# Kernel tuning notes

Measured on AMD Instinct MI355X. Metric: run time of the kernel, lower is better.

The kernel has to match this reference:

```python
import jax, jax.numpy as jnp
import numpy as np

N_IN, M_MID = 512, 256
B, H, W = 16, 64, 64

def setup_inputs() -> dict:
    key = jax.random.key(0)
    ks = jax.random.split(key, 7)
    s = 0.05
    return {
        "x": jax.random.normal(ks[0], (B, N_IN, H, W), dtype=jnp.float32),
        "W_state": jax.random.normal(ks[1], (M_MID, N_IN), dtype=jnp.float32) * s,
        "b_state": jax.random.normal(ks[2], (M_MID,), dtype=jnp.float32) * s,
        "W_proj": jax.random.normal(ks[3], (M_MID, N_IN), dtype=jnp.float32) * s,
        "b_proj": jax.random.normal(ks[4], (M_MID,), dtype=jnp.float32) * s,
        "W_extend": jax.random.normal(ks[5], (N_IN, M_MID), dtype=jnp.float32) * s,
        "b_extend": jax.random.normal(ks[6], (N_IN,), dtype=jnp.float32) * s,
    }

def reference(x, W_state, b_state, W_proj, b_proj, W_extend, b_extend):
    n, c, h, w = x.shape
    hw = h * w
    xf = x.reshape(n, c, hw)                                   # [n, C, HW]
    # 1x1 convs are channel GEMMs over flattened spatial dim
    x_state = jnp.einsum('mc,nch->nmh', W_state, xf) + b_state[None, :, None]   # [n, M, HW]
    x_proj = jnp.einsum('mc,nch->nmh', W_proj, xf) + b_proj[None, :, None]      # [n, M, HW]
    # bmm -> scale -> softmax -> bmm (graph reasoning over M x M)
    scores = jnp.einsum('nmh,nkh->nmk', x_state, x_proj) / jnp.sqrt(jnp.float32(hw))
    attn = jax.nn.softmax(scores, axis=2)                      # [n, M, M]
    x_rstate = jnp.einsum('nmk,nkh->nmh', attn, x_proj)        # [n, M, HW]
    # extend back to C channels + residual
    ext = jnp.einsum('cm,nmh->nch', W_extend, x_rstate) + b_extend[None, :, None]
    return x + ext.reshape(n, c, h, w)
```

## Files before the change

### kernel.cpp

```cpp
#include <hip/hip_runtime.h>
#include <hip/hip_bf16.h>
#include <stdint.h>

typedef __bf16 bf16x8_t __attribute__((ext_vector_type(8)));
typedef float  f32x4_t  __attribute__((ext_vector_type(4)));
typedef short  short8_t __attribute__((ext_vector_type(8)));

__device__ __forceinline__ unsigned short f2b(float f) {
    union { float f; unsigned u; } v; v.f = f;
    unsigned u = v.u;
    return (unsigned short)((u + 0x7FFFu + ((u >> 16) & 1u)) >> 16);
}
__device__ __forceinline__ float b2f(unsigned short b) {
    union { unsigned u; float f; } v; v.u = ((unsigned)b) << 16; return v.f;
}

#define AS3(p) ((__attribute__((address_space(3))) void*)(p))
#define AS1(p) ((const __attribute__((address_space(1))) void*)(p))
#define FENCE() asm volatile("" ::: "memory")

#define NB   16
#define CIN  512
#define MMID 256
#define HW   4096
#define KSPLIT 8
#define ASZ  (128 * 64)
#define ASZ2 (256 * 64)

__device__ __forceinline__ void swz3(int gx, int gy, int& bx, int& by, int& bz) {
    const int nwg = gridDim.x, ord = blockIdx.x, q = nwg >> 3;
    const int s = (ord & 7) * q + (ord >> 3);
    by = s % gy;
    const int rem = s / gy;
    bx = rem % gx;
    bz = rem / gx;
}

__global__ __launch_bounds__(256) void prep_weights(
    const float* __restrict__ Ws, const float* __restrict__ Wp,
    const float* __restrict__ Wef, const float* __restrict__ bs,
    const float* __restrict__ bp,
    unsigned short* __restrict__ Wsp, unsigned short* __restrict__ Wex,
    unsigned short* __restrict__ WpT, float* __restrict__ bsp)
{
    int i = blockIdx.x * 256 + threadIdx.x;
    if (i < MMID * CIN) {
        Wsp[i]              = f2b(Ws[i]);
        Wsp[MMID * CIN + i] = f2b(Wp[i]);
        Wex[i]              = f2b(Wef[i]);
        const int c = i >> 8, k = i & (MMID - 1);
        WpT[i] = f2b(Wp[(size_t)k * CIN + c]);
    }
    if (i < MMID) { bsp[i] = bs[i]; bsp[MMID + i] = bp[i]; }
}

__global__ __launch_bounds__(256) void transpose_convert_x(
    const float* __restrict__ x, unsigned short* __restrict__ xT)
{
    __shared__ unsigned short tile[64][66];
    const int n = blockIdx.z, c0 = blockIdx.y * 64, h0 = blockIdx.x * 64;
    const float* s = x + ((size_t)n * CIN + c0) * HW + h0;
    unsigned short* d = xT + ((size_t)n * HW + h0) * CIN + c0;
    const int t = threadIdx.x;
    {
        const int rr = t >> 4, cc = (t & 15) * 4;
        #pragma unroll
        for (int p = 0; p < 4; ++p) {
            int r = p * 16 + rr;
            float4 v = *(const float4*)(s + (size_t)r * HW + cc);
            tile[r][cc + 0] = f2b(v.x); tile[r][cc + 1] = f2b(v.y);
            tile[r][cc + 2] = f2b(v.z); tile[r][cc + 3] = f2b(v.w);
        }
    }
    __syncthreads();
    {
        const int wr = t >> 3, wc = (t & 7) * 8;
        #pragma unroll
        for (int p = 0; p < 2; ++p) {
            int h = p * 32 + wr;
            unsigned short tmp[8];
            #pragma unroll
            for (int j = 0; j < 8; ++j) tmp[j] = tile[wc + j][h];
            *(short8_t*)(d + (size_t)h * CIN + wc) = *(const short8_t*)tmp;
        }
    }
}

__global__ __launch_bounds__(256) void transpose_bf16_64(
    const unsigned short* __restrict__ src, unsigned short* __restrict__ dst,
    int srs, int drs, long long sbs, long long dbs)
{
    __shared__ unsigned short tile[64][66];
    const int n = blockIdx.z, r0 = blockIdx.y * 64, c0 = blockIdx.x * 64;
    const unsigned short* s = src + (size_t)n * sbs + (size_t)r0 * srs + c0;
    unsigned short* d = dst + (size_t)n * dbs + (size_t)c0 * drs + r0;
    const int t = threadIdx.x;
    const int rr = t >> 3, cc = (t & 7) * 8;
    #pragma unroll
    for (int p = 0; p < 2; ++p) {
        int r = p * 32 + rr;
        short8_t v = *(const short8_t*)(s + (size_t)r * srs + cc);
        #pragma unroll
        for (int j = 0; j < 8; ++j) tile[r][cc + j] = ((const unsigned short*)&v)[j];
    }
    __syncthreads();
    #pragma unroll
    for (int p = 0; p < 2; ++p) {
        int c = p * 32 + rr;
        unsigned short tmp[8];
        #pragma unroll
        for (int j = 0; j < 8; ++j) tmp[j] = tile[cc + j][c];
        *(short8_t*)(d + (size_t)c * drs + cc) = *(const short8_t*)tmp;
    }
}

template <int EPI>
__device__ __forceinline__ void epilogue_repack(
    f32x4_t (&acc)[4][4], unsigned short* smem,
    int m0, int n0, int wave, int lane,
    const float* __restrict__ bias, const float* __restrict__ resid,
    void* __restrict__ Cout, int ldc, size_t cbase)
{
    float* fbuf = (float*)smem;
    const int t   = wave * 64 + lane;
    const int l15 = lane & 15, l16 = lane >> 4;
    const int wr2 = wave >> 1;
    const int wc  = (wave & 1) * 64;

    #pragma unroll
    for (int p = 0; p < 4; ++p) {
        __syncthreads();
        if (wr2 == (p >> 1)) {
            const int ihalf = p & 1;
            #pragma unroll
            for (int i2 = 0; i2 < 2; ++i2) {
                const int i = ihalf * 2 + i2;
                #pragma unroll
                for (int r = 0; r < 4; ++r) {
                    const int lrow = i2 * 16 + l16 * 4 + r;
                    #pragma unroll
                    for (int j = 0; j < 4; ++j)
                        fbuf[lrow * 132 + wc + j * 16 + l15] = acc[i][j][r];
                }
            }
        }
        __syncthreads();
        #pragma unroll
        for (int it = 0; it < 2; ++it) {
            const int lrow = it * 16 + (t >> 4);
            const int col  = (t & 15) * 8;
            const int row  = m0 + p * 32 + lrow;
            float v[8];
            *(float4*)&v[0] = *(const float4*)&fbuf[lrow * 132 + col];
            *(float4*)&v[4] = *(const float4*)&fbuf[lrow * 132 + col + 4];
            float badd = 0.f;
            if constexpr (EPI == 0 || EPI == 3) badd = bias[row];
            const size_t idx = cbase + (size_t)row * ldc + n0 + col;
            if constexpr (EPI == 3) {
                float o[8];
                const float* rp = resid + idx;
                float4 r0 = *(const float4*)rp;
                float4 r1 = *(const float4*)(rp + 4);
                o[0] = v[0] + badd + r0.x; o[1] = v[1] + badd + r0.y;
                o[2] = v[2] + badd + r0.z; o[3] = v[3] + badd + r0.w;
                o[4] = v[4] + badd + r1.x; o[5] = v[5] + badd + r1.y;
                o[6] = v[6] + badd + r1.z; o[7] = v[7] + badd + r1.w;
                float* op = (float*)Cout + idx;
                *(float4*)op = *(const float4*)&o[0];
                *(float4*)(op + 4) = *(const float4*)&o[4];
            } else if constexpr (EPI == 1) {
                float* op = (float*)Cout + idx;
                *(float4*)op = *(const float4*)&v[0];
                *(float4*)(op + 4) = *(const float4*)&v[4];
            } else {
                unsigned short o[8];
                #pragma unroll
                for (int k = 0; k < 8; ++k) o[k] = f2b(v[k] + badd);
                *(short8_t*)((unsigned short*)Cout + idx) = *(const short8_t*)o;
            }
        }
    }
}

#define GEMM_KLOOP(Ab, Bb, lda, ldb, KBEG, NT)                                          \
    auto stage = [&](int k0, int b) {                                                   \
        unsigned short* Asb = smem + b * 2 * ASZ;                                       \
        unsigned short* Bsb = Asb + ASZ;                                                \
        _Pragma("unroll")                                                               \
        for (int c = 0; c < 4; ++c) {                                                   \
            const int o   = (c * 256 + t) * 16;                                         \
            const int row = o >> 7;                                                     \
            const int ce  = ((o & 127) ^ ((row & 7) << 4)) >> 1;                        \
            __builtin_amdgcn_global_load_lds(                                           \
                AS1(Ab + (size_t)row * lda + k0 + ce), AS3((char*)Asb + o), 16, 0, 0);  \
            __builtin_amdgcn_global_load_lds(                                           \
                AS1(Bb + (size_t)row * ldb + k0 + ce), AS3((char*)Bsb + o), 16, 0, 0);  \
        }                                                                               \
    };                                                                                  \
    stage(KBEG, 0);                                                                     \
    for (int itk = 0; itk < (NT); ++itk) {                                              \
        const int cur = itk & 1;                                                        \
        if (itk + 1 < (NT)) {                                                           \
            stage(KBEG + (itk + 1) * 64, cur ^ 1);                                      \
            asm volatile("s_waitcnt vmcnt(8)" ::: "memory");                            \
        } else {                                                                        \
            asm volatile("s_waitcnt vmcnt(0)" ::: "memory");                            \
        }                                                                               \
        __builtin_amdgcn_s_barrier();                                                   \
        FENCE();                                                                        \
        const char* Asb = (const char*)(smem + cur * 2 * ASZ);                          \
        const char* Bsb = Asb + 2 * ASZ;                                                \
        const int swz = (l15 & 7) << 4;                                                 \
        _Pragma("unroll")                                                               \
        for (int ks = 0; ks < 2; ++ks) {                                                \
            bf16x8_t af[4], bfr[4];                                                     \
            const int cb = (ks * 64 + l16 * 16) ^ swz;                                  \
            _Pragma("unroll")                                                           \
            for (int i = 0; i < 4; ++i) {                                               \
                af[i]  = *(const bf16x8_t*)(Asb + (wr + i * 16 + l15) * 128 + cb);      \
                bfr[i] = *(const bf16x8_t*)(Bsb + (wc + i * 16 + l15) * 128 + cb);      \
            }                                                                           \
            _Pragma("unroll")                                                           \
            for (int i = 0; i < 4; ++i)                                                 \
                _Pragma("unroll")                                                       \
                for (int j = 0; j < 4; ++j)                                             \
                    acc[i][j] = __builtin_amdgcn_mfma_f32_16x16x32_bf16(                \
                        af[i], bfr[j], acc[i][j], 0, 0, 0);                             \
        }                                                                               \
        FENCE();                                                                        \
        __builtin_amdgcn_s_barrier();                                                   \
        FENCE();                                                                        \
    }

template <int EPI>
__global__ __launch_bounds__(512, 2) void gemm256(
    const unsigned short* __restrict__ A, const unsigned short* __restrict__ B,
    int lda, int ldb, int K,
    long long strideA, long long strideB,
    const float* __restrict__ bias, int bias_bstride,
    const float* __restrict__ resid,
    void* __restrict__ Cout, int ldc, long long strideC,
    int gx, int gy)
{
    __shared__ unsigned short smem[4 * ASZ2];

    int bx, by, n;  swz3(gx, gy, bx, by, n);
    const int m0 = by * 256;
    const int n0 = bx * 256;

    const unsigned short* Ab = A + (size_t)n * strideA + (size_t)m0 * lda;
    const unsigned short* Bb = B + (size_t)n * strideB + (size_t)n0 * ldb;

    const int t    = threadIdx.x;
    const int lane = t & 63;
    const int wave = t >> 6;
    const int wr2  = wave >> 2;
    const int wc4  = wave & 3;
    const int l15  = lane & 15;
    const int l16  = lane >> 4;

    f32x4_t acc[8][4] = {};

    auto stage = [&](int k0, int b) {
        unsigned short* Asb = smem + b * 2 * ASZ2;
        unsigned short* Bsb = Asb + ASZ2;
        #pragma unroll
        for (int c = 0; c < 4; ++c) {
            const int o   = (c * 512 + t) * 16;
            const int row = o >> 7;
            const int ce  = ((o & 127) ^ ((row & 7) << 4)) >> 1;
            __builtin_amdgcn_global_load_lds(
                AS1(Ab + (size_t)row * lda + k0 + ce), AS3((char*)Asb + o), 16, 0, 0);
            __builtin_amdgcn_global_load_lds(
                AS1(Bb + (size_t)row * ldb + k0 + ce), AS3((char*)Bsb + o), 16, 0, 0);
        }
    };

    const int NT = K / 64;
    stage(0, 0);
    for (int itk = 0; itk < NT; ++itk) {
        const int cur = itk & 1;
        if (itk + 1 < NT) {
            stage((itk + 1) * 64, cur ^ 1);
            asm volatile("s_waitcnt vmcnt(8)" ::: "memory");
        } else {
            asm volatile("s_waitcnt vmcnt(0)" ::: "memory");
        }
        __builtin_amdgcn_s_barrier();
        FENCE();
        const char* Asb = (const char*)(smem + cur * 2 * ASZ2);
        const char* Bsb = Asb + 2 * ASZ2;
        const int swz = (l15 & 7) << 4;
        #pragma unroll
        for (int ks = 0; ks < 2; ++ks) {
            const int cb = (ks * 64 + l16 * 16) ^ swz;
            bf16x8_t af[8], bfr[4];
            #pragma unroll
            for (int i = 0; i < 8; ++i)
                af[i] = *(const bf16x8_t*)(Asb + (wr2 * 128 + i * 16 + l15) * 128 + cb);
            #pragma unroll
            for (int j = 0; j < 4; ++j)
                bfr[j] = *(const bf16x8_t*)(Bsb + (wc4 * 64 + j * 16 + l15) * 128 + cb);
            #pragma unroll
            for (int i = 0; i < 8; ++i)
                #pragma unroll
                for (int j = 0; j < 4; ++j)
                    acc[i][j] = __builtin_amdgcn_mfma_f32_16x16x32_bf16(
                        af[i], bfr[j], acc[i][j], 0, 0, 0);
        }
        FENCE();
        __builtin_amdgcn_s_barrier();
        FENCE();
    }

    float* fbuf = (float*)smem;
    const size_t cbase = (size_t)n * strideC;
    const float* beff = bias ? bias + (size_t)n * bias_bstride : nullptr;
    #pragma unroll
    for (int p = 0; p < 8; ++p) {
        __syncthreads();
        if (wr2 == (p >> 2)) {
            #pragma unroll
            for (int i2 = 0; i2 < 2; ++i2) {
                const int i = (p & 3) * 2 + i2;
                #pragma unroll
                for (int r = 0; r < 4; ++r) {
                    const int lrow = i2 * 16 + l16 * 4 + r;
                    #pragma unroll
                    for (int j = 0; j < 4; ++j)
                        fbuf[lrow * 264 + wc4 * 64 + j * 16 + l15] = acc[i][j][r];
                }
            }
        }
        __syncthreads();
        #pragma unroll
        for (int it = 0; it < 2; ++it) {
            const int lrow = it * 16 + (t >> 5);
            const int col  = (t & 31) * 8;
            const int row  = m0 + p * 32 + lrow;
            float v[8];
            *(float4*)&v[0] = *(const float4*)&fbuf[lrow * 264 + col];
            *(float4*)&v[4] = *(const float4*)&fbuf[lrow * 264 + col + 4];
            const float badd = beff ? beff[row] : 0.f;
            const size_t idx = cbase + (size_t)row * ldc + n0 + col;
            if constexpr (EPI == 3) {
                float o[8];
                const float* rp = resid + idx;
                float4 r0 = *(const float4*)rp;
                float4 r1 = *(const float4*)(rp + 4);
                o[0] = v[0] + badd + r0.x; o[1] = v[1] + badd + r0.y;
                o[2] = v[2] + badd + r0.z; o[3] = v[3] + badd + r0.w;
                o[4] = v[4] + badd + r1.x; o[5] = v[5] + badd + r1.y;
                o[6] = v[6] + badd + r1.z; o[7] = v[7] + badd + r1.w;
                float* op = (float*)Cout + idx;
                *(float4*)op = *(const float4*)&o[0];
                *(float4*)(op + 4) = *(const float4*)&o[4];
            } else {
                unsigned short o[8];
                #pragma unroll
                for (int k = 0; k < 8; ++k) o[k] = f2b(v[k] + badd);
                *(short8_t*)((unsigned short*)Cout + idx) = *(const short8_t*)o;
            }
        }
    }
}

__global__ __launch_bounds__(256) void gemm_scores(
    const unsigned short* __restrict__ Ysp, float* __restrict__ scoresP)
{
    __shared__ unsigned short smem[4 * ASZ];

    int bx, by, z;  swz3(MMID / 128, MMID / 128, bx, by, z);
    const int n  = z >> 3;
    const int kc = z & 7;
    const int m0 = by * 128;
    const int n0 = bx * 128;

    const unsigned short* Ab = Ysp + (size_t)n * CIN * HW + (size_t)m0 * HW;
    const unsigned short* Bb = Ysp + (size_t)n * CIN * HW + (size_t)(MMID + n0) * HW;

    const int t    = threadIdx.x;
    const int lane = t & 63;
    const int wave = t >> 6;
    const int wr   = (wave >> 1) * 64;
    const int wc   = (wave & 1) * 64;
    const int l15  = lane & 15;
    const int l16  = lane >> 4;

    f32x4_t acc[4][4] = {};
    const int kbeg = kc * (HW / KSPLIT);
    GEMM_KLOOP(Ab, Bb, HW, HW, kbeg, (HW / KSPLIT) / 64)

    float* outp = scoresP + (size_t)(kc * NB + n) * MMID * MMID;
    epilogue_repack<1>(acc, smem, m0, n0, wave, lane, nullptr, nullptr,
                       outp, MMID, 0);
}

__global__ __launch_bounds__(256) void softmax_rows(
    const float* __restrict__ scoresP, unsigned short* __restrict__ attn)
{
    const int wave = threadIdx.x >> 6;
    const int l    = threadIdx.x & 63;
    const size_t row = (size_t)blockIdx.x * 4 + wave;
    const size_t pstride = (size_t)NB * MMID * MMID;
    float4 v = {0.f, 0.f, 0.f, 0.f};
    #pragma unroll
    for (int p = 0; p < KSPLIT; ++p) {
        float4 u = *(const float4*)(scoresP + p * pstride + row * MMID + l * 4);
        v.x += u.x; v.y += u.y; v.z += u.z; v.w += u.w;
    }
    float mx = fmaxf(fmaxf(v.x, v.y), fmaxf(v.z, v.w));
    #pragma unroll
    for (int off = 32; off; off >>= 1) mx = fmaxf(mx, __shfl_xor(mx, off));
    const float sc = 0.015625f;
    float e0 = __expf((v.x - mx) * sc), e1 = __expf((v.y - mx) * sc);
    float e2 = __expf((v.z - mx) * sc), e3 = __expf((v.w - mx) * sc);
    float sum = e0 + e1 + e2 + e3;
    #pragma unroll
    for (int off = 32; off; off >>= 1) sum += __shfl_xor(sum, off);
    const float inv = 1.0f / sum;
    unsigned short o[4] = { f2b(e0 * inv), f2b(e1 * inv), f2b(e2 * inv), f2b(e3 * inv) };
    *(uint64_t*)(attn + row * MMID + l * 4) = *(const uint64_t*)o;
}

__global__ __launch_bounds__(256) void compute_vec(
    const unsigned short* __restrict__ G, const float* __restrict__ bsp,
    const float* __restrict__ be, float* __restrict__ vec)
{
    const int n = blockIdx.x >> 1;
    const int c = ((blockIdx.x & 1) << 8) + threadIdx.x;
    const unsigned short* g = G + ((size_t)n * CIN + c) * MMID;
    float s = 0.f;
    for (int k = 0; k < MMID; k += 8) {
        short8_t v = *(const short8_t*)(g + k);
        #pragma unroll
        for (int j = 0; j < 8; ++j)
            s += b2f((unsigned short)v[j]) * bsp[MMID + k + j];
    }
    vec[n * CIN + c] = be[c] + s;
}

template <int EPI>
__global__ __launch_bounds__(256) void gemm_nt(
    const unsigned short* __restrict__ A, const unsigned short* __restrict__ B,
    int lda, int ldb, int K,
    long long strideA, long long strideB,
    const float* __restrict__ bias, int bias_bstride,
    const float* __restrict__ resid,
    void* __restrict__ Cout, int ldc, long long strideC,
    int gx, int gy)
{
    __shared__ unsigned short smem[4 * ASZ];

    int bx, by, n;  swz3(gx, gy, bx, by, n);
    const int m0 = by * 128;
    const int n0 = bx * 128;

    const unsigned short* Ab = A + (size_t)n * strideA + (size_t)m0 * lda;
    const unsigned short* Bb = B + (size_t)n * strideB + (size_t)n0 * ldb;

    const int t    = threadIdx.x;
    const int lane = t & 63;
    const int wave = t >> 6;
    const int wr   = (wave >> 1) * 64;
    const int wc   = (wave & 1) * 64;
    const int l15  = lane & 15;
    const int l16  = lane >> 4;

    f32x4_t acc[4][4] = {};
    GEMM_KLOOP(Ab, Bb, lda, ldb, 0, K / 64)

    const float* beff = bias ? bias + (size_t)n * bias_bstride : nullptr;
    epilogue_repack<EPI>(acc, smem, m0, n0, wave, lane, beff, resid,
                         Cout, ldc, (size_t)n * strideC);
}

extern "C" void kernel_launch(void* const* d_in, const int* in_sizes, int n_in,
                              void* d_out, int out_size, void* d_ws, size_t ws_size,
                              hipStream_t stream)
{
    const float* x   = (const float*)d_in[0];
    const float* Ws  = (const float*)d_in[1];
    const float* bs  = (const float*)d_in[2];
    const float* Wp  = (const float*)d_in[3];
    const float* bp  = (const float*)d_in[4];
    const float* Wef = (const float*)d_in[5];
    const float* be  = (const float*)d_in[6];
    float* out = (float*)d_out;

    unsigned short* xT   = (unsigned short*)d_ws;
    unsigned short* Ysp  = xT   + (size_t)NB * HW * CIN;
    unsigned short* Wsp  = Ysp  + (size_t)NB * CIN * HW;
    unsigned short* Wex  = Wsp  + (size_t)CIN * CIN;
    unsigned short* WpT  = Wex  + (size_t)CIN * MMID;
    unsigned short* attn = WpT  + (size_t)CIN * MMID;
    unsigned short* attnT= attn + (size_t)NB * MMID * MMID;
    unsigned short* G    = attnT+ (size_t)NB * MMID * MMID;
    unsigned short* Meff = G    + (size_t)NB * CIN * MMID;
    float* scoresP = (float*)(Meff + (size_t)NB * CIN * CIN);
    float* bsp = scoresP + (size_t)KSPLIT * NB * MMID * MMID;
    float* vec = bsp + CIN;

    prep_weights<<<512, 256, 0, stream>>>(Ws, Wp, Wef, bs, bp, Wsp, Wex, WpT, bsp);

    transpose_convert_x<<<dim3(HW / 64, CIN / 64, NB), 256, 0, stream>>>(x, xT);

    gemm256<0><<<(HW / 256) * (CIN / 256) * NB, 512, 0, stream>>>(
        Wsp, xT, CIN, CIN, CIN,
        0LL, (long long)HW * CIN,
        bsp, 0, nullptr, Ysp, HW, (long long)CIN * HW,
        HW / 256, CIN / 256);

    gemm_scores<<<(MMID / 128) * (MMID / 128) * NB * KSPLIT, 256, 0, stream>>>(
        Ysp, scoresP);

    softmax_rows<<<NB * MMID / 4, 256, 0, stream>>>(scoresP, attn);

    transpose_bf16_64<<<dim3(MMID / 64, MMID / 64, NB), 256, 0, stream>>>(
        attn, attnT, MMID, MMID, (long long)MMID * MMID, (long long)MMID * MMID);

    gemm_nt<2><<<(MMID / 128) * (CIN / 128) * NB, 256, 0, stream>>>(
        Wex, attnT, MMID, MMID, MMID,
        0LL, (long long)MMID * MMID,
        nullptr, 0, nullptr, G, MMID, (long long)CIN * MMID,
        MMID / 128, CIN / 128);

    compute_vec<<<NB * 2, 256, 0, stream>>>(G, bsp, be, vec);

    gemm_nt<2><<<(CIN / 128) * (CIN / 128) * NB, 256, 0, stream>>>(
        G, WpT, MMID, MMID, MMID,
        (long long)CIN * MMID, 0LL,
        nullptr, 0, nullptr, Meff, CIN, (long long)CIN * CIN,
        CIN / 128, CIN / 128);

    gemm256<3><<<(HW / 256) * (CIN / 256) * NB, 512, 0, stream>>>(
        Meff, xT, CIN, CIN, CIN,
        (long long)CIN * CIN, (long long)HW * CIN,
        vec, CIN, x, out, HW, (long long)CIN * HW,
        HW / 256, CIN / 256);
}
```

Baseline: 224.2 us.

## Use full-M 512x128 GEMM tiles and fold residual into identity-augmented Meff

Replaces the 256x256 batched GEMM with a 512x128 tile that covers the whole output-channel dimension, so each block streams its xT column tile only once. The residual add is moved into the effective matrix by adding the identity in the Meff epilogue, which removes the fp32 x read from the final GEMM epilogue. The score GEMM split-K is also halved. In exchange the residual now passes through bf16 (Meff+I rounded, xT in bf16), which lowers accuracy, and occupancy drops to one block per CU because of the larger LDS footprint.

```diff
diff --git a/kernel.cpp b/kernel.cpp
--- a/kernel.cpp
+++ b/kernel.cpp
@@ -23,9 +23,10 @@
 #define CIN  512
 #define MMID 256
 #define HW   4096
-#define KSPLIT 8
+#define KSPLIT 4
 #define ASZ  (128 * 64)
-#define ASZ2 (256 * 64)
+#define ASZA (512 * 64)
+#define ASZB (128 * 64)
 
 __device__ __forceinline__ void swz3(int gx, int gy, int& bx, int& by, int& bz) {
     const int nwg = gridDim.x, ord = blockIdx.x, q = nwg >> 3;
@@ -118,7 +119,6 @@
 __device__ __forceinline__ void epilogue_repack(
     f32x4_t (&acc)[4][4], unsigned short* smem,
     int m0, int n0, int wave, int lane,
-    const float* __restrict__ bias, const float* __restrict__ resid,
     void* __restrict__ Cout, int ldc, size_t cbase)
 {
     float* fbuf = (float*)smem;
@@ -153,29 +153,21 @@
             float v[8];
             *(float4*)&v[0] = *(const float4*)&fbuf[lrow * 132 + col];
             *(float4*)&v[4] = *(const float4*)&fbuf[lrow * 132 + col + 4];
-            float badd = 0.f;
-            if constexpr (EPI == 0 || EPI == 3) badd = bias[row];
             const size_t idx = cbase + (size_t)row * ldc + n0 + col;
-            if constexpr (EPI == 3) {
-                float o[8];
-                const float* rp = resid + idx;
-                float4 r0 = *(const float4*)rp;
-                float4 r1 = *(const float4*)(rp + 4);
-                o[0] = v[0] + badd + r0.x; o[1] = v[1] + badd + r0.y;
-                o[2] = v[2] + badd + r0.z; o[3] = v[3] + badd + r0.w;
-                o[4] = v[4] + badd + r1.x; o[5] = v[5] + badd + r1.y;
-                o[6] = v[6] + badd + r1.z; o[7] = v[7] + badd + r1.w;
-                float* op = (float*)Cout + idx;
-                *(float4*)op = *(const float4*)&o[0];
-                *(float4*)(op + 4) = *(const float4*)&o[4];
-            } else if constexpr (EPI == 1) {
+            if constexpr (EPI == 1) {
                 float* op = (float*)Cout + idx;
                 *(float4*)op = *(const float4*)&v[0];
                 *(float4*)(op + 4) = *(const float4*)&v[4];
+            } else if constexpr (EPI == 4) {
+                unsigned short o[8];
+                #pragma unroll
+                for (int k = 0; k < 8; ++k)
+                    o[k] = f2b(v[k] + ((row == n0 + col + k) ? 1.0f : 0.0f));
+                *(short8_t*)((unsigned short*)Cout + idx) = *(const short8_t*)o;
             } else {
                 unsigned short o[8];
                 #pragma unroll
-                for (int k = 0; k < 8; ++k) o[k] = f2b(v[k] + badd);
+                for (int k = 0; k < 8; ++k) o[k] = f2b(v[k]);
                 *(short8_t*)((unsigned short*)Cout + idx) = *(const short8_t*)o;
             }
         }
@@ -233,63 +225,65 @@
     }
 
 template <int EPI>
-__global__ __launch_bounds__(512, 2) void gemm256(
+__global__ __launch_bounds__(512, 1) void gemm512(
     const unsigned short* __restrict__ A, const unsigned short* __restrict__ B,
-    int lda, int ldb, int K,
     long long strideA, long long strideB,
     const float* __restrict__ bias, int bias_bstride,
-    const float* __restrict__ resid,
-    void* __restrict__ Cout, int ldc, long long strideC,
-    int gx, int gy)
-{
-    __shared__ unsigned short smem[4 * ASZ2];
-
-    int bx, by, n;  swz3(gx, gy, bx, by, n);
-    const int m0 = by * 256;
-    const int n0 = bx * 256;
-
-    const unsigned short* Ab = A + (size_t)n * strideA + (size_t)m0 * lda;
-    const unsigned short* Bb = B + (size_t)n * strideB + (size_t)n0 * ldb;
+    void* __restrict__ Cout, int ldc, long long strideC, int gx)
+{
+    __shared__ unsigned short smem[2 * (ASZA + ASZB)];
+
+    int bx, by, n;  swz3(gx, 1, bx, by, n);
+    const int n0 = bx * 128;
+
+    const unsigned short* Ab = A + (size_t)n * strideA;
+    const unsigned short* Bb = B + (size_t)n * strideB + (size_t)n0 * CIN;
 
     const int t    = threadIdx.x;
     const int lane = t & 63;
     const int wave = t >> 6;
-    const int wr2  = wave >> 2;
-    const int wc4  = wave & 3;
+    const int wr   = (wave >> 1) * 128;
+    const int wc   = (wave & 1) * 64;
     const int l15  = lane & 15;
     const int l16  = lane >> 4;
 
     f32x4_t acc[8][4] = {};
 
     auto stage = [&](int k0, int b) {
-        unsigned short* Asb = smem + b * 2 * ASZ2;
-        unsigned short* Bsb = Asb + ASZ2;
-        #pragma unroll
-        for (int c = 0; c < 4; ++c) {
+        unsigned short* Asb = smem + b * (ASZA + ASZB);
+        unsigned short* Bsb = Asb + ASZA;
+        #pragma unroll
+        for (int c = 0; c < 8; ++c) {
             const int o   = (c * 512 + t) * 16;
             const int row = o >> 7;
             const int ce  = ((o & 127) ^ ((row & 7) << 4)) >> 1;
             __builtin_amdgcn_global_load_lds(
-                AS1(Ab + (size_t)row * lda + k0 + ce), AS3((char*)Asb + o), 16, 0, 0);
+                AS1(Ab + (size_t)row * CIN + k0 + ce), AS3((char*)Asb + o), 16, 0, 0);
+        }
+        #pragma unroll
+        for (int c = 0; c < 2; ++c) {
+            const int o   = (c * 512 + t) * 16;
+            const int row = o >> 7;
+            const int ce  = ((o & 127) ^ ((row & 7) << 4)) >> 1;
             __builtin_amdgcn_global_load_lds(
-                AS1(Bb + (size_t)row * ldb + k0 + ce), AS3((char*)Bsb + o), 16, 0, 0);
+                AS1(Bb + (size_t)row * CIN + k0 + ce), AS3((char*)Bsb + o), 16, 0, 0);
         }
     };
 
-    const int NT = K / 64;
+    const int NT = CIN / 64;
     stage(0, 0);
     for (int itk = 0; itk < NT; ++itk) {
         const int cur = itk & 1;
         if (itk + 1 < NT) {
             stage((itk + 1) * 64, cur ^ 1);
-            asm volatile("s_waitcnt vmcnt(8)" ::: "memory");
+            asm volatile("s_waitcnt vmcnt(10)" ::: "memory");
         } else {
             asm volatile("s_waitcnt vmcnt(0)" ::: "memory");
         }
         __builtin_amdgcn_s_barrier();
         FENCE();
-        const char* Asb = (const char*)(smem + cur * 2 * ASZ2);
-        const char* Bsb = Asb + 2 * ASZ2;
+        const char* Asb = (const char*)(smem + cur * (ASZA + ASZB));
+        const char* Bsb = Asb + 2 * ASZA;
         const int swz = (l15 & 7) << 4;
         #pragma unroll
         for (int ks = 0; ks < 2; ++ks) {
@@ -297,10 +291,10 @@
             bf16x8_t af[8], bfr[4];
             #pragma unroll
             for (int i = 0; i < 8; ++i)
-                af[i] = *(const bf16x8_t*)(Asb + (wr2 * 128 + i * 16 + l15) * 128 + cb);
+                af[i] = *(const bf16x8_t*)(Asb + (wr + i * 16 + l15) * 128 + cb);
             #pragma unroll
             for (int j = 0; j < 4; ++j)
-                bfr[j] = *(const bf16x8_t*)(Bsb + (wc4 * 64 + j * 16 + l15) * 128 + cb);
+                bfr[j] = *(const bf16x8_t*)(Bsb + (wc + j * 16 + l15) * 128 + cb);
             #pragma unroll
             for (int i = 0; i < 8; ++i)
                 #pragma unroll
@@ -315,11 +309,11 @@
 
     float* fbuf = (float*)smem;
     const size_t cbase = (size_t)n * strideC;
-    const float* beff = bias ? bias + (size_t)n * bias_bstride : nullptr;
-    #pragma unroll
-    for (int p = 0; p < 8; ++p) {
+    const float* beff = bias + (size_t)n * bias_bstride;
+    #pragma unroll
+    for (int p = 0; p < 16; ++p) {
         __syncthreads();
-        if (wr2 == (p >> 2)) {
+        if ((wave >> 1) == (p >> 2)) {
             #pragma unroll
             for (int i2 = 0; i2 < 2; ++i2) {
                 const int i = (p & 3) * 2 + i2;
@@ -328,39 +322,31 @@
                     const int lrow = i2 * 16 + l16 * 4 + r;
                     #pragma unroll
                     for (int j = 0; j < 4; ++j)
-                        fbuf[lrow * 264 + wc4 * 64 + j * 16 + l15] = acc[i][j][r];
+                        fbuf[lrow * 132 + wc + j * 16 + l15] = acc[i][j][r];
                 }
             }
         }
         __syncthreads();
-        #pragma unroll
-        for (int it = 0; it < 2; ++it) {
-            const int lrow = it * 16 + (t >> 5);
-            const int col  = (t & 31) * 8;
-            const int row  = m0 + p * 32 + lrow;
-            float v[8];
-            *(float4*)&v[0] = *(const float4*)&fbuf[lrow * 264 + col];
-            *(float4*)&v[4] = *(const float4*)&fbuf[lrow * 264 + col + 4];
-            const float badd = beff ? beff[row] : 0.f;
-            const size_t idx = cbase + (size_t)row * ldc + n0 + col;
-            if constexpr (EPI == 3) {
-                float o[8];
-                const float* rp = resid + idx;
-                float4 r0 = *(const float4*)rp;
-                float4 r1 = *(const float4*)(rp + 4);
-                o[0] = v[0] + badd + r0.x; o[1] = v[1] + badd + r0.y;
-                o[2] = v[2] + badd + r0.z; o[3] = v[3] + badd + r0.w;
-                o[4] = v[4] + badd + r1.x; o[5] = v[5] + badd + r1.y;
-                o[6] = v[6] + badd + r1.z; o[7] = v[7] + badd + r1.w;
-                float* op = (float*)Cout + idx;
-                *(float4*)op = *(const float4*)&o[0];
-                *(float4*)(op + 4) = *(const float4*)&o[4];
-            } else {
-                unsigned short o[8];
-                #pragma unroll
-                for (int k = 0; k < 8; ++k) o[k] = f2b(v[k] + badd);
-                *(short8_t*)((unsigned short*)Cout + idx) = *(const short8_t*)o;
-            }
+        const int lrow = t >> 4;
+        const int col  = (t & 15) * 8;
+        const int row  = p * 32 + lrow;
+        float v[8];
+        *(float4*)&v[0] = *(const float4*)&fbuf[lrow * 132 + col];
+        *(float4*)&v[4] = *(const float4*)&fbuf[lrow * 132 + col + 4];
+        const float badd = beff[row];
+        const size_t idx = cbase + (size_t)row * ldc + n0 + col;
+        if constexpr (EPI == 1) {
+            float o[8];
+            #pragma unroll
+            for (int k = 0; k < 8; ++k) o[k] = v[k] + badd;
+            float* op = (float*)Cout + idx;
+            *(float4*)op = *(const float4*)&o[0];
+            *(float4*)(op + 4) = *(const float4*)&o[4];
+        } else {
+            unsigned short o[8];
+            #pragma unroll
+            for (int k = 0; k < 8; ++k) o[k] = f2b(v[k] + badd);
+            *(short8_t*)((unsigned short*)Cout + idx) = *(const short8_t*)o;
         }
     }
 }
@@ -371,8 +357,8 @@
     __shared__ unsigned short smem[4 * ASZ];
 
     int bx, by, z;  swz3(MMID / 128, MMID / 128, bx, by, z);
-    const int n  = z >> 3;
-    const int kc = z & 7;
+    const int n  = z >> 2;
+    const int kc = z & 3;
     const int m0 = by * 128;
     const int n0 = bx * 128;
 
@@ -392,8 +378,7 @@
     GEMM_KLOOP(Ab, Bb, HW, HW, kbeg, (HW / KSPLIT) / 64)
 
     float* outp = scoresP + (size_t)(kc * NB + n) * MMID * MMID;
-    epilogue_repack<1>(acc, smem, m0, n0, wave, lane, nullptr, nullptr,
-                       outp, MMID, 0);
+    epilogue_repack<1>(acc, smem, m0, n0, wave, lane, outp, MMID, 0);
 }
 
 __global__ __launch_bounds__(256) void softmax_rows(
@@ -445,8 +430,6 @@
     const unsigned short* __restrict__ A, const unsigned short* __restrict__ B,
     int lda, int ldb, int K,
     long long strideA, long long strideB,
-    const float* __restrict__ bias, int bias_bstride,
-    const float* __restrict__ resid,
     void* __restrict__ Cout, int ldc, long long strideC,
     int gx, int gy)
 {
@@ -470,8 +453,7 @@
     f32x4_t acc[4][4] = {};
     GEMM_KLOOP(Ab, Bb, lda, ldb, 0, K / 64)
 
-    const float* beff = bias ? bias + (size_t)n * bias_bstride : nullptr;
-    epilogue_repack<EPI>(acc, smem, m0, n0, wave, lane, beff, resid,
+    epilogue_repack<EPI>(acc, smem, m0, n0, wave, lane,
                          Cout, ldc, (size_t)n * strideC);
 }
 
@@ -505,11 +487,9 @@
 
     transpose_convert_x<<<dim3(HW / 64, CIN / 64, NB), 256, 0, stream>>>(x, xT);
 
-    gemm256<0><<<(HW / 256) * (CIN / 256) * NB, 512, 0, stream>>>(
-        Wsp, xT, CIN, CIN, CIN,
-        0LL, (long long)HW * CIN,
-        bsp, 0, nullptr, Ysp, HW, (long long)CIN * HW,
-        HW / 256, CIN / 256);
+    gemm512<0><<<(HW / 128) * NB, 512, 0, stream>>>(
+        Wsp, xT, 0LL, (long long)HW * CIN,
+        bsp, 0, Ysp, HW, (long long)CIN * HW, HW / 128);
 
     gemm_scores<<<(MMID / 128) * (MMID / 128) * NB * KSPLIT, 256, 0, stream>>>(
         Ysp, scoresP);
@@ -522,20 +502,18 @@
     gemm_nt<2><<<(MMID / 128) * (CIN / 128) * NB, 256, 0, stream>>>(
         Wex, attnT, MMID, MMID, MMID,
         0LL, (long long)MMID * MMID,
-        nullptr, 0, nullptr, G, MMID, (long long)CIN * MMID,
+        G, MMID, (long long)CIN * MMID,
         MMID / 128, CIN / 128);
 
     compute_vec<<<NB * 2, 256, 0, stream>>>(G, bsp, be, vec);
 
-    gemm_nt<2><<<(CIN / 128) * (CIN / 128) * NB, 256, 0, stream>>>(
+    gemm_nt<4><<<(CIN / 128) * (CIN / 128) * NB, 256, 0, stream>>>(
         G, WpT, MMID, MMID, MMID,
         (long long)CIN * MMID, 0LL,
-        nullptr, 0, nullptr, Meff, CIN, (long long)CIN * CIN,
+        Meff, CIN, (long long)CIN * CIN,
         CIN / 128, CIN / 128);
 
-    gemm256<3><<<(HW / 256) * (CIN / 256) * NB, 512, 0, stream>>>(
-        Meff, xT, CIN, CIN, CIN,
-        (long long)CIN * CIN, (long long)HW * CIN,
-        vec, CIN, x, out, HW, (long long)CIN * HW,
-        HW / 256, CIN / 256);
-}
+    gemm512<1><<<(HW / 128) * NB, 512, 0, stream>>>(
+        Meff, xT, (long long)CIN * CIN, (long long)HW * CIN,
+        vec, CIN, out, HW, (long long)CIN * HW, HW / 128);
+}
```

Result: faster. 206.4 us (-7.9%).
